# Kernel tuning notes

Measured on AMD Instinct MI355X. Metric: run time of the kernel, lower is better.

## Reference

```python
import jax, jax.numpy as jnp
import numpy as np


def _prelu(x, a):
    return jnp.where(x >= 0, x, a * x)


def _conv1x1(x, w, b, a):
    # x: [N,C,H,W], w: [O,C], b: [O] -> PReLU(conv1x1(x))
    y = jnp.einsum('oc,nchw->nohw', w, x) + b[None, :, None, None]
    return _prelu(y, a)


def setup_inputs() -> dict:
    key = jax.random.key(0)
    ks = jax.random.split(key, 8)
    N, C, H, W = 4, 128, 64, 64
    Cr = C // 2  # reduction=2
    sC = 1.0 / np.sqrt(C)
    x = jax.random.normal(ks[0], (N, C, H, W), dtype=jnp.float32)
    w1 = jax.random.normal(ks[1], (Cr, C), dtype=jnp.float32) * sC
    b1 = jnp.zeros((Cr,), dtype=jnp.float32)
    a1 = jnp.asarray(0.25, dtype=jnp.float32)  # PReLU (single shared slope)
    w2 = jax.random.normal(ks[2], (Cr, C), dtype=jnp.float32) * sC
    b2 = jnp.zeros((Cr,), dtype=jnp.float32)
    a2 = jnp.asarray(0.25, dtype=jnp.float32)
    wa = jax.random.normal(ks[3], (C, C), dtype=jnp.float32) * sC
    ba = jnp.zeros((C,), dtype=jnp.float32)
    aa = jnp.asarray(0.25, dtype=jnp.float32)
    return {"x": x, "w1": w1, "b1": b1, "a1": a1,
            "w2": w2, "b2": b2, "a2": a2,
            "wa": wa, "ba": ba, "aa": aa}


def reference(x, w1, b1, a1, w2, b2, a2, wa, ba, aa):
    N, C, H, W = x.shape
    HW = H * W
    e1 = _conv1x1(x, w1, b1, a1).reshape(N, -1, HW)   # [N,Cr,HW]
    e2 = _conv1x1(x, w2, b2, a2).reshape(N, -1, HW)   # [N,Cr,HW]
    asm = _conv1x1(x, wa, ba, aa).reshape(N, C, HW)   # [N,C,HW]
    # ksize=1: per-channel outer products summed over channels == single contraction
    score = jnp.einsum('nci,ncj->nij', e1, e2)        # [N,HW,HW]
    score = jax.nn.softmax(score, axis=2)
    out = jnp.einsum('nij,ncj->nci', score, asm)      # [N,C,HW]
    return out.reshape(N, C, H, W)
```

## Files before the change

kernel.cpp:

```cpp
#include <hip/hip_runtime.h>
#include <hip/hip_bf16.h>
#include <stdint.h>


typedef float   f32x16 __attribute__((ext_vector_type(16)));
typedef __bf16  bf16x8 __attribute__((ext_vector_type(8)));
typedef __bf16  bf16x2 __attribute__((ext_vector_type(2)));
typedef unsigned int u32x4 __attribute__((ext_vector_type(4)));
typedef unsigned int u32x2 __attribute__((ext_vector_type(2)));

#define L2E 1.4426950408889634f

#define Q_OFF   (0u)
#define KF_OFF  (2u << 20)
#define VF_OFF  (4u << 20)
#define DEN_OFF (8u << 20)
#define WH_OFF  ((8u << 20) + (1u << 19))
#define WL_OFF  (WH_OFF + (1u << 16))
#define OP_OFF  (9u << 20)

__device__ inline unsigned short f2bf(float f) {
  __bf16 h = (__bf16)f;
  return __builtin_bit_cast(unsigned short, h);
}
__device__ inline float bf2f(unsigned short h) {
  unsigned u = ((unsigned)h) << 16;
  return __builtin_bit_cast(float, u);
}
__device__ inline unsigned pack2(float a, float b) {
  bf16x2 t = { (__bf16)a, (__bf16)b };
  return __builtin_bit_cast(unsigned, t);
}

__device__ inline void gld_lds16(const void* g, void* l) {
  __builtin_amdgcn_global_load_lds(
      (const __attribute__((address_space(1))) unsigned*)g,
      (__attribute__((address_space(3))) unsigned*)l, 16, 0, 0);
}

__global__ void wcast_kernel(const float* __restrict__ w1, const float* __restrict__ w2,
                             const float* __restrict__ wa, char* __restrict__ ws) {
  int idx = blockIdx.x * 256 + threadIdx.x;
  unsigned short* WH = (unsigned short*)(ws + WH_OFF);
  unsigned short* WL = (unsigned short*)(ws + WL_OFF);
#pragma unroll
  for (int r = 0; r < 4; ++r) {
    int i = r * 8192 + idx;
    int oc = i >> 7, c = i & 127;
    float v = oc < 64 ? w1[oc * 128 + c]
            : (oc < 128 ? w2[(oc - 64) * 128 + c] : wa[(oc - 128) * 128 + c]);
    __bf16 h = (__bf16)v;
    WH[i] = __builtin_bit_cast(unsigned short, h);
    WL[i] = f2bf(v - (float)h);
  }
}

__global__ __launch_bounds__(256) void conv_kernel(
    const float* __restrict__ x, char* __restrict__ ws,
    const float* __restrict__ b1, const float* __restrict__ a1,
    const float* __restrict__ b2, const float* __restrict__ a2,
    const float* __restrict__ ba, const float* __restrict__ aa) {
  int bid = blockIdx.x;
  int n = bid >> 7, st = bid & 127;
  int sb = st * 32;
  int tid = threadIdx.x;
  int wid = tid >> 6, lane = tid & 63, l31 = lane & 31, hi = lane >> 5;

  __shared__ float xl[128][36];
  __shared__ float tl[2][64][33];
  float* vl = (float*)xl;

  const float* xb = x + (size_t)n * 128 * 4096;
#pragma unroll
  for (int it = 0; it < 4; ++it) {
    int flat4 = tid + 256 * it;
    int c = flat4 >> 3, s4 = flat4 & 7;
    float4 v = *(const float4*)(xb + (size_t)c * 4096 + sb + s4 * 4);
    *(float4*)&xl[c][s4 * 4] = v;
  }
  __syncthreads();

  const char* WH = ws + WH_OFF;
  const char* WL = ws + WL_OFF;
  int oc0 = wid * 64;

  f32x16 acc[2];
  acc[0] = 0.f; acc[1] = 0.f;
#pragma unroll
  for (int c0 = 0; c0 < 8; ++c0) {
    __bf16 eh[8], el[8];
#pragma unroll
    for (int j = 0; j < 8; ++j) {
      float v = xl[c0 * 16 + hi * 8 + j][l31];
      __bf16 h = (__bf16)v;
      eh[j] = h;
      el[j] = (__bf16)(v - (float)h);
    }
    bf16x8 xh = {eh[0], eh[1], eh[2], eh[3], eh[4], eh[5], eh[6], eh[7]};
    bf16x8 xlo = {el[0], el[1], el[2], el[3], el[4], el[5], el[6], el[7]};
#pragma unroll
    for (int mb = 0; mb < 2; ++mb) {
      size_t wo = (size_t)(oc0 + mb * 32 + l31) * 256 + c0 * 32 + hi * 16;
      bf16x8 wh = *(const bf16x8*)(WH + wo);
      bf16x8 wl = *(const bf16x8*)(WL + wo);
      acc[mb] = __builtin_amdgcn_mfma_f32_32x32x16_bf16(wh, xh, acc[mb], 0, 0, 0);
      acc[mb] = __builtin_amdgcn_mfma_f32_32x32x16_bf16(wh, xlo, acc[mb], 0, 0, 0);
      acc[mb] = __builtin_amdgcn_mfma_f32_32x32x16_bf16(wl, xh, acc[mb], 0, 0, 0);
    }
  }
  __syncthreads();

  if (wid < 2) {
    const float* bb = wid ? b2 : b1;
    float slope = wid ? a2[0] : a1[0];
    float scl = wid ? 1.0f : L2E;
#pragma unroll
    for (int mb = 0; mb < 2; ++mb)
#pragma unroll
      for (int reg = 0; reg < 16; ++reg) {
        int row = mb * 32 + (reg & 3) + 8 * (reg >> 2) + 4 * hi;
        float y = acc[mb][reg] + bb[row];
        y = fmaxf(y, 0.f) + slope * fminf(y, 0.f);
        tl[wid][row][l31] = y * scl;
      }
  } else {
    float slope = aa[0];
#pragma unroll
    for (int mb = 0; mb < 2; ++mb)
#pragma unroll
      for (int reg = 0; reg < 16; ++reg) {
        int dv = (wid - 2) * 64 + mb * 32 + (reg & 3) + 8 * (reg >> 2) + 4 * hi;
        float y = acc[mb][reg] + ba[dv];
        y = fmaxf(y, 0.f) + slope * fminf(y, 0.f);
        vl[dv * 33 + l31] = y;
      }
  }
  __syncthreads();

  if (wid == 0) {
    char* Qg = ws + Q_OFF + (size_t)n * (4096 * 128);
#pragma unroll
    for (int it = 0; it < 4; ++it) {
      int sl = (lane >> 3) + it * 8;
      u32x4 pv;
#pragma unroll
      for (int p = 0; p < 4; ++p)
        pv[p] = pack2(tl[0][(lane & 7) * 8 + 2 * p][sl],
                      tl[0][(lane & 7) * 8 + 2 * p + 1][sl]);
      *(u32x4*)(Qg + (size_t)(sb + sl) * 128 + (lane & 7) * 16) = pv;
    }
  } else if (wid == 1) {
    char* KFb = ws + KF_OFF + (size_t)n * (512 << 10);
    int d0 = (lane & 7) >> 1, hs = lane & 1;
#pragma unroll
    for (int it = 0; it < 4; ++it) {
      int sl = (lane >> 3) + it * 8;
      u32x4 pv;
#pragma unroll
      for (int p = 0; p < 4; ++p)
        pv[p] = pack2(tl[1][(lane & 7) * 8 + 2 * p][sl],
                      tl[1][(lane & 7) * 8 + 2 * p + 1][sl]);
      *(u32x4*)(KFb + ((size_t)(st * 4 + d0) * 64 + hs * 32 + sl) * 16) = pv;
    }
  }
  {
    char* VFb = ws + VF_OFF + (size_t)n * (1u << 20);
#pragma unroll
    for (int r = 0; r < 2; ++r) {
      int u = tid + r * 256;
      int dv = u >> 2, sc = u & 3;
      u32x4 pv;
#pragma unroll
      for (int p = 0; p < 4; ++p)
        pv[p] = pack2(vl[dv * 33 + sc * 8 + 2 * p], vl[dv * 33 + sc * 8 + 2 * p + 1]);
      int unit = st * 8 + (dv >> 5) * 2 + (sc >> 1);
      *(u32x4*)(VFb + ((size_t)unit * 64 + (sc & 1) * 32 + (dv & 31)) * 16) = pv;
    }
  }
}

__global__ __launch_bounds__(256, 2) void attn_kernel(char* __restrict__ ws) {
  int bid = blockIdx.x;
  int split = bid & 3;
  int qt = (bid >> 2) & 15;
  int batch = bid >> 6;
  int tid = threadIdx.x;
  int wid = tid >> 6, lane = tid & 63, l31 = lane & 31, hi = lane >> 5;

  const char* Qb  = ws + Q_OFF  + (size_t)batch * (4096 * 128);
  const char* Kt0 = ws + KF_OFF + (size_t)batch * (512 << 10) +
                    (size_t)(split * 32) * 4096;
  const char* Vt0 = ws + VF_OFF + (size_t)batch * (1u << 20) +
                    (size_t)(split * 32) * 8192;

  __shared__ char sbuf[3][12288];

  int q0 = qt * 256 + wid * 64;
  int lo16 = lane * 16;

  bf16x8 qf0[4], qf1[4];
#pragma unroll
  for (int d0 = 0; d0 < 4; ++d0) {
    qf0[d0] = *(const bf16x8*)(Qb + (size_t)(q0 + l31) * 128 + d0 * 32 + hi * 16);
    qf1[d0] = *(const bf16x8*)(Qb + (size_t)(q0 + 32 + l31) * 128 + d0 * 32 + hi * 16);
  }

  f32x16 oacc[2][4];
#pragma unroll
  for (int qs = 0; qs < 2; ++qs)
#pragma unroll
    for (int i = 0; i < 4; ++i) oacc[qs][i] = 0.f;
  float denA0 = 0.f, denA1 = 0.f, denB0 = 0.f, denB1 = 0.f;

  auto stage = [&](int b, int t) {
#pragma unroll
    for (int i = 0; i < 3; ++i) {
      int c = wid * 3 + i;
      const char* src = (c < 4) ? Kt0 + (size_t)t * 4096 + c * 1024 + lo16
                                : Vt0 + (size_t)t * 8192 + (c - 4) * 1024 + lo16;
      gld_lds16(src, &sbuf[b][c * 1024]);
    }
  };

  stage(0, 0);
  stage(1, 1);

  for (int t = 0; t < 32; ++t) {
    if (t < 31) asm volatile("s_waitcnt vmcnt(3)" ::: "memory");
    else        asm volatile("s_waitcnt vmcnt(0)" ::: "memory");
    __builtin_amdgcn_s_barrier();

    if (t + 2 < 32) stage((t + 2) % 3, t + 2);

    const char* kb = sbuf[t % 3];
    const char* vb = kb + 4096;

    f32x16 s0, s1;
    s0 = 0.f; s1 = 0.f;
#pragma unroll
    for (int d0 = 0; d0 < 4; ++d0) {
      bf16x8 kf = *(const bf16x8*)(kb + d0 * 1024 + lo16);
      s0 = __builtin_amdgcn_mfma_f32_32x32x16_bf16(kf, qf0[d0], s0, 0, 0, 0);
      s1 = __builtin_amdgcn_mfma_f32_32x32x16_bf16(kf, qf1[d0], s1, 0, 0, 0);
    }

    unsigned pk0[8], pk1[8];
#pragma unroll
    for (int m = 0; m < 8; ++m) {
      float a0 = __builtin_amdgcn_exp2f(s0[2 * m]);
      float a1 = __builtin_amdgcn_exp2f(s0[2 * m + 1]);
      if (m & 1) denA1 += a0 + a1; else denA0 += a0 + a1;
      pk0[m] = pack2(a0, a1);
      float b0 = __builtin_amdgcn_exp2f(s1[2 * m]);
      float b1 = __builtin_amdgcn_exp2f(s1[2 * m + 1]);
      if (m & 1) denB1 += b0 + b1; else denB0 += b0 + b1;
      pk1[m] = pack2(b0, b1);
    }

#pragma unroll
    for (int kc = 0; kc < 2; ++kc) {
      const int bs = kc * 4;
      u32x2 r0 = __builtin_amdgcn_permlane32_swap(pk0[bs + 0], pk0[bs + 2],
                                                  false, false);
      u32x2 r1 = __builtin_amdgcn_permlane32_swap(pk0[bs + 1], pk0[bs + 3],
                                                  false, false);
      u32x4 pu0 = {r0.x, r1.x, r0.y, r1.y};
      bf16x8 pf0 = __builtin_bit_cast(bf16x8, pu0);
      u32x2 r2 = __builtin_amdgcn_permlane32_swap(pk1[bs + 0], pk1[bs + 2],
                                                  false, false);
      u32x2 r3 = __builtin_amdgcn_permlane32_swap(pk1[bs + 1], pk1[bs + 3],
                                                  false, false);
      u32x4 pu1 = {r2.x, r3.x, r2.y, r3.y};
      bf16x8 pf1 = __builtin_bit_cast(bf16x8, pu1);
#pragma unroll
      for (int dvb = 0; dvb < 4; ++dvb) {
        bf16x8 vf = *(const bf16x8*)(vb + (dvb * 2 + kc) * 1024 + lo16);
        oacc[0][dvb] = __builtin_amdgcn_mfma_f32_32x32x16_bf16(vf, pf0,
                                                               oacc[0][dvb], 0, 0, 0);
        oacc[1][dvb] = __builtin_amdgcn_mfma_f32_32x32x16_bf16(vf, pf1,
                                                               oacc[1][dvb], 0, 0, 0);
      }
    }
  }

  unsigned short* OPu = (unsigned short*)(ws + OP_OFF) +
                        (size_t)((batch * 16 + qt) * 4 + split) * 32768;
#pragma unroll
  for (int qs = 0; qs < 2; ++qs) {
    int qloc = wid * 64 + qs * 32 + l31;
#pragma unroll
    for (int dvb = 0; dvb < 4; ++dvb)
#pragma unroll
      for (int reg = 0; reg < 16; ++reg) {
        int dv = dvb * 32 + (reg & 3) + 8 * (reg >> 2) + 4 * hi;
        OPu[dv * 256 + qloc] = f2bf(oacc[qs][dvb][reg]);
      }
    float den = qs ? (denB0 + denB1) : (denA0 + denA1);
    float dtot = den + __shfl_xor(den, 32, 64);
    if (hi == 0) {
      float* DEN = (float*)(ws + DEN_OFF) +
                   (size_t)((batch * 16 + qt) * 4 + split) * 256;
      DEN[qloc] = dtot;
    }
  }
}

__global__ __launch_bounds__(256) void combine_kernel(const char* __restrict__ ws,
                                                      float* __restrict__ out) {
  int idx8 = (blockIdx.x * 256 + threadIdx.x) * 8;
  int n = idx8 >> 19;
  int dv = (idx8 >> 12) & 127;
  int s0 = idx8 & 4095;
  int qt = s0 >> 8, ql = s0 & 255;
  const unsigned short* OPu = (const unsigned short*)(ws + OP_OFF);
  const float* DEN = (const float*)(ws + DEN_OFF);
  size_t pb = (size_t)((n * 16 + qt) * 4);
  float num[8], den[8];
#pragma unroll
  for (int j = 0; j < 8; ++j) { num[j] = 0.f; den[j] = 0.f; }
#pragma unroll
  for (int h = 0; h < 4; ++h) {
    bf16x8 v = *(const bf16x8*)(OPu + (pb + h) * 32768 + (size_t)dv * 256 + ql);
    const float* dp = DEN + (pb + h) * 256 + ql;
    float4 d0 = *(const float4*)dp;
    float4 d1 = *(const float4*)(dp + 4);
#pragma unroll
    for (int j = 0; j < 8; ++j) num[j] += (float)v[j];
    den[0] += d0.x; den[1] += d0.y; den[2] += d0.z; den[3] += d0.w;
    den[4] += d1.x; den[5] += d1.y; den[6] += d1.z; den[7] += d1.w;
  }
  float4 o0 = {num[0] / den[0], num[1] / den[1], num[2] / den[2], num[3] / den[3]};
  float4 o1 = {num[4] / den[4], num[5] / den[5], num[6] / den[6], num[7] / den[7]};
  *(float4*)&out[idx8] = o0;
  *(float4*)&out[idx8 + 4] = o1;
}

extern "C" void kernel_launch(void* const* d_in, const int* in_sizes, int n_in,
                              void* d_out, int out_size, void* d_ws, size_t ws_size,
                              hipStream_t stream) {
  (void)in_sizes; (void)n_in; (void)out_size; (void)ws_size;
  const float* x  = (const float*)d_in[0];
  const float* w1 = (const float*)d_in[1];
  const float* b1 = (const float*)d_in[2];
  const float* a1 = (const float*)d_in[3];
  const float* w2 = (const float*)d_in[4];
  const float* b2 = (const float*)d_in[5];
  const float* a2 = (const float*)d_in[6];
  const float* wa = (const float*)d_in[7];
  const float* ba = (const float*)d_in[8];
  const float* aa = (const float*)d_in[9];
  char* ws = (char*)d_ws;
  float* out = (float*)d_out;

  wcast_kernel<<<dim3(32), dim3(256), 0, stream>>>(w1, w2, wa, ws);
  conv_kernel<<<dim3(512), dim3(256), 0, stream>>>(x, ws, b1, a1, b2, a2, ba, aa);
  attn_kernel<<<dim3(256), dim3(256), 0, stream>>>(ws);
  combine_kernel<<<dim3(1024), dim3(256), 0, stream>>>(ws, out);
}
```

Measured before the change: 59.29 us.

## Fuse split-K combine into attention kernel via last-block atomic counter

Removes the separate combine kernel launch. Each attention block atomically increments a per-(batch,qtile) counter after writing its partial output, and the last of the four split blocks reduces the partials and normalizes by the summed denominators directly into the output. This saves a kernel launch and its tail, at the cost of a memset for the counters and a serialized reduction inside the last-arriving block, which may lengthen the attention kernel's tail.

New measurement: 148.5 us. 150% more time.

```diff
diff --git a/kernel.cpp b/kernel.cpp
--- a/kernel.cpp
+++ b/kernel.cpp
@@ -15,6 +15,7 @@
 #define KF_OFF  (2u << 20)
 #define VF_OFF  (4u << 20)
 #define DEN_OFF (8u << 20)
+#define CNT_OFF ((8u << 20) + (256u << 10))
 #define WH_OFF  ((8u << 20) + (1u << 19))
 #define WL_OFF  (WH_OFF + (1u << 16))
 #define OP_OFF  (9u << 20)
@@ -179,7 +180,8 @@
   }
 }
 
-__global__ __launch_bounds__(256, 2) void attn_kernel(char* __restrict__ ws) {
+__global__ __launch_bounds__(256, 2) void attn_kernel(char* __restrict__ ws,
+                                                      float* __restrict__ out) {
   int bid = blockIdx.x;
   int split = bid & 3;
   int qt = (bid >> 2) & 15;
@@ -194,6 +196,7 @@
                     (size_t)(split * 32) * 8192;
 
   __shared__ char sbuf[3][12288];
+  __shared__ int lastFlag;
 
   int q0 = qt * 256 + wid * 64;
   int lo16 = lane * 16;
@@ -283,8 +286,9 @@
     }
   }
 
+  int grp = batch * 16 + qt;
   unsigned short* OPu = (unsigned short*)(ws + OP_OFF) +
-                        (size_t)((batch * 16 + qt) * 4 + split) * 32768;
+                        (size_t)(grp * 4 + split) * 32768;
 #pragma unroll
   for (int qs = 0; qs < 2; ++qs) {
     int qloc = wid * 64 + qs * 32 + l31;
@@ -298,41 +302,49 @@
     float den = qs ? (denB0 + denB1) : (denA0 + denA1);
     float dtot = den + __shfl_xor(den, 32, 64);
     if (hi == 0) {
-      float* DEN = (float*)(ws + DEN_OFF) +
-                   (size_t)((batch * 16 + qt) * 4 + split) * 256;
+      float* DEN = (float*)(ws + DEN_OFF) + (size_t)(grp * 4 + split) * 256;
       DEN[qloc] = dtot;
     }
   }
-}
-
-__global__ __launch_bounds__(256) void combine_kernel(const char* __restrict__ ws,
-                                                      float* __restrict__ out) {
-  int idx8 = (blockIdx.x * 256 + threadIdx.x) * 8;
-  int n = idx8 >> 19;
-  int dv = (idx8 >> 12) & 127;
-  int s0 = idx8 & 4095;
-  int qt = s0 >> 8, ql = s0 & 255;
-  const unsigned short* OPu = (const unsigned short*)(ws + OP_OFF);
-  const float* DEN = (const float*)(ws + DEN_OFF);
-  size_t pb = (size_t)((n * 16 + qt) * 4);
-  float num[8], den[8];
-#pragma unroll
-  for (int j = 0; j < 8; ++j) { num[j] = 0.f; den[j] = 0.f; }
-#pragma unroll
-  for (int h = 0; h < 4; ++h) {
-    bf16x8 v = *(const bf16x8*)(OPu + (pb + h) * 32768 + (size_t)dv * 256 + ql);
-    const float* dp = DEN + (pb + h) * 256 + ql;
-    float4 d0 = *(const float4*)dp;
-    float4 d1 = *(const float4*)(dp + 4);
-#pragma unroll
-    for (int j = 0; j < 8; ++j) num[j] += (float)v[j];
-    den[0] += d0.x; den[1] += d0.y; den[2] += d0.z; den[3] += d0.w;
-    den[4] += d1.x; den[5] += d1.y; den[6] += d1.z; den[7] += d1.w;
-  }
-  float4 o0 = {num[0] / den[0], num[1] / den[1], num[2] / den[2], num[3] / den[3]};
-  float4 o1 = {num[4] / den[4], num[5] / den[5], num[6] / den[6], num[7] / den[7]};
-  *(float4*)&out[idx8] = o0;
-  *(float4*)&out[idx8 + 4] = o1;
+
+  __threadfence();
+  if (tid == 0) {
+    unsigned* cnt = (unsigned*)(ws + CNT_OFF);
+    unsigned old = atomicAdd(&cnt[grp], 1u);
+    lastFlag = (old == 3u) ? 1 : 0;
+  }
+  __syncthreads();
+  if (lastFlag) {
+    __threadfence();
+    const unsigned short* OPg = (const unsigned short*)(ws + OP_OFF) +
+                                (size_t)grp * 4 * 32768;
+    const float* DENg = (const float*)(ws + DEN_OFF) + (size_t)grp * 4 * 256;
+    int dv = tid >> 1;
+    int qlb = (tid & 1) * 128;
+    float* og = out + ((size_t)batch * 128 + dv) * 4096 + qt * 256 + qlb;
+#pragma unroll
+    for (int u = 0; u < 16; ++u) {
+      int ql = qlb + u * 8;
+      float num[8], den[8];
+#pragma unroll
+      for (int j = 0; j < 8; ++j) { num[j] = 0.f; den[j] = 0.f; }
+#pragma unroll
+      for (int sp = 0; sp < 4; ++sp) {
+        bf16x8 v = *(const bf16x8*)(OPg + sp * 32768 + dv * 256 + ql);
+        const float* dp = DENg + sp * 256 + ql;
+        float4 d0 = *(const float4*)dp;
+        float4 d1 = *(const float4*)(dp + 4);
+#pragma unroll
+        for (int j = 0; j < 8; ++j) num[j] += (float)v[j];
+        den[0] += d0.x; den[1] += d0.y; den[2] += d0.z; den[3] += d0.w;
+        den[4] += d1.x; den[5] += d1.y; den[6] += d1.z; den[7] += d1.w;
+      }
+      float4 o0 = {num[0] / den[0], num[1] / den[1], num[2] / den[2], num[3] / den[3]};
+      float4 o1 = {num[4] / den[4], num[5] / den[5], num[6] / den[6], num[7] / den[7]};
+      *(float4*)(og + u * 8) = o0;
+      *(float4*)(og + u * 8 + 4) = o1;
+    }
+  }
 }
 
 extern "C" void kernel_launch(void* const* d_in, const int* in_sizes, int n_in,
@@ -352,8 +364,8 @@
   char* ws = (char*)d_ws;
   float* out = (float*)d_out;
 
+  hipMemsetAsync(ws + CNT_OFF, 0, 64 * sizeof(unsigned), stream);
   wcast_kernel<<<dim3(32), dim3(256), 0, stream>>>(w1, w2, wa, ws);
   conv_kernel<<<dim3(512), dim3(256), 0, stream>>>(x, ws, b1, a1, b2, a2, ba, aa);
-  attn_kernel<<<dim3(256), dim3(256), 0, stream>>>(ws);
-  combine_kernel<<<dim3(1024), dim3(256), 0, stream>>>(ws, out);
-}
+  attn_kernel<<<dim3(256), dim3(256), 0, stream>>>(ws, out);
+}
```

## Split keys across warps within a block and fuse the combine step into attention

Applied to the files above, without the earlier changes.

Each block now covers one 64-query tile. Its four warps each process a quarter of the key range with private triple-buffered LDS staging, so the per-iteration block barrier goes away. The partial numerators and denominators are reduced through shared memory at the end, and the normalized output is written directly. This removes the separate combine kernel launch and the global round-trip of bf16 partials. In exchange the kernel uses 144KB of LDS, so occupancy drops to one block per CU with only four waves. Each warp also issues its own K/V loads, which quadruples LDS fill traffic per block.

Result: slower. 61.08 us (+3.0%).

```diff
diff --git a/kernel.cpp b/kernel.cpp
--- a/kernel.cpp
+++ b/kernel.cpp
@@ -14,10 +14,8 @@
 #define Q_OFF   (0u)
 #define KF_OFF  (2u << 20)
 #define VF_OFF  (4u << 20)
-#define DEN_OFF (8u << 20)
 #define WH_OFF  ((8u << 20) + (1u << 19))
 #define WL_OFF  (WH_OFF + (1u << 16))
-#define OP_OFF  (9u << 20)
 
 __device__ inline unsigned short f2bf(float f) {
   __bf16 h = (__bf16)f;
@@ -179,23 +177,24 @@
   }
 }
 
-__global__ __launch_bounds__(256, 2) void attn_kernel(char* __restrict__ ws) {
+__global__ __launch_bounds__(256, 1) void attn_kernel(char* __restrict__ ws,
+                                                      float* __restrict__ out) {
   int bid = blockIdx.x;
-  int split = bid & 3;
-  int qt = (bid >> 2) & 15;
-  int batch = bid >> 6;
+  int batch = bid & 3;
+  int qt = bid >> 2;
   int tid = threadIdx.x;
   int wid = tid >> 6, lane = tid & 63, l31 = lane & 31, hi = lane >> 5;
 
   const char* Qb  = ws + Q_OFF  + (size_t)batch * (4096 * 128);
   const char* Kt0 = ws + KF_OFF + (size_t)batch * (512 << 10) +
-                    (size_t)(split * 32) * 4096;
+                    (size_t)(wid * 32) * 4096;
   const char* Vt0 = ws + VF_OFF + (size_t)batch * (1u << 20) +
-                    (size_t)(split * 32) * 8192;
-
-  __shared__ char sbuf[3][12288];
-
-  int q0 = qt * 256 + wid * 64;
+                    (size_t)(wid * 32) * 8192;
+
+  __shared__ char sbuf[4][3][12288];
+  char* myb = &sbuf[wid][0][0];
+
+  int q0 = qt * 64;
   int lo16 = lane * 16;
 
   bf16x8 qf0[4], qf1[4];
@@ -213,26 +212,26 @@
   float denA0 = 0.f, denA1 = 0.f, denB0 = 0.f, denB1 = 0.f;
 
   auto stage = [&](int b, int t) {
-#pragma unroll
-    for (int i = 0; i < 3; ++i) {
-      int c = wid * 3 + i;
-      const char* src = (c < 4) ? Kt0 + (size_t)t * 4096 + c * 1024 + lo16
-                                : Vt0 + (size_t)t * 8192 + (c - 4) * 1024 + lo16;
-      gld_lds16(src, &sbuf[b][c * 1024]);
-    }
+    char* dst = myb + b * 12288;
+    const char* ks = Kt0 + (size_t)t * 4096;
+    const char* vs = Vt0 + (size_t)t * 8192;
+#pragma unroll
+    for (int i = 0; i < 4; ++i) gld_lds16(ks + i * 1024 + lo16, dst + i * 1024);
+#pragma unroll
+    for (int i = 0; i < 8; ++i) gld_lds16(vs + i * 1024 + lo16,
+                                          dst + 4096 + i * 1024);
   };
 
   stage(0, 0);
   stage(1, 1);
 
   for (int t = 0; t < 32; ++t) {
-    if (t < 31) asm volatile("s_waitcnt vmcnt(3)" ::: "memory");
+    if (t < 31) asm volatile("s_waitcnt vmcnt(12)" ::: "memory");
     else        asm volatile("s_waitcnt vmcnt(0)" ::: "memory");
-    __builtin_amdgcn_s_barrier();
 
     if (t + 2 < 32) stage((t + 2) % 3, t + 2);
 
-    const char* kb = sbuf[t % 3];
+    const char* kb = myb + (t % 3) * 12288;
     const char* vb = kb + 4096;
 
     f32x16 s0, s1;
@@ -283,56 +282,49 @@
     }
   }
 
-  unsigned short* OPu = (unsigned short*)(ws + OP_OFF) +
-                        (size_t)((batch * 16 + qt) * 4 + split) * 32768;
+  __syncthreads();
+
+  unsigned short* pOP = (unsigned short*)&sbuf[0][0][0];
+  float* pDEN = (float*)((char*)pOP + 4 * 64 * 136 * 2);
+
 #pragma unroll
   for (int qs = 0; qs < 2; ++qs) {
-    int qloc = wid * 64 + qs * 32 + l31;
+    int q = qs * 32 + l31;
 #pragma unroll
     for (int dvb = 0; dvb < 4; ++dvb)
 #pragma unroll
-      for (int reg = 0; reg < 16; ++reg) {
-        int dv = dvb * 32 + (reg & 3) + 8 * (reg >> 2) + 4 * hi;
-        OPu[dv * 256 + qloc] = f2bf(oacc[qs][dvb][reg]);
+      for (int j = 0; j < 4; ++j) {
+        int db = dvb * 32 + 8 * j + 4 * hi;
+        u32x2 wv = { pack2(oacc[qs][dvb][4 * j],     oacc[qs][dvb][4 * j + 1]),
+                     pack2(oacc[qs][dvb][4 * j + 2], oacc[qs][dvb][4 * j + 3]) };
+        *(u32x2*)&pOP[(wid * 64 + q) * 136 + db] = wv;
       }
     float den = qs ? (denB0 + denB1) : (denA0 + denA1);
     float dtot = den + __shfl_xor(den, 32, 64);
-    if (hi == 0) {
-      float* DEN = (float*)(ws + DEN_OFF) +
-                   (size_t)((batch * 16 + qt) * 4 + split) * 256;
-      DEN[qloc] = dtot;
-    }
-  }
-}
-
-__global__ __launch_bounds__(256) void combine_kernel(const char* __restrict__ ws,
-                                                      float* __restrict__ out) {
-  int idx8 = (blockIdx.x * 256 + threadIdx.x) * 8;
-  int n = idx8 >> 19;
-  int dv = (idx8 >> 12) & 127;
-  int s0 = idx8 & 4095;
-  int qt = s0 >> 8, ql = s0 & 255;
-  const unsigned short* OPu = (const unsigned short*)(ws + OP_OFF);
-  const float* DEN = (const float*)(ws + DEN_OFF);
-  size_t pb = (size_t)((n * 16 + qt) * 4);
-  float num[8], den[8];
-#pragma unroll
-  for (int j = 0; j < 8; ++j) { num[j] = 0.f; den[j] = 0.f; }
-#pragma unroll
-  for (int h = 0; h < 4; ++h) {
-    bf16x8 v = *(const bf16x8*)(OPu + (pb + h) * 32768 + (size_t)dv * 256 + ql);
-    const float* dp = DEN + (pb + h) * 256 + ql;
-    float4 d0 = *(const float4*)dp;
-    float4 d1 = *(const float4*)(dp + 4);
-#pragma unroll
-    for (int j = 0; j < 8; ++j) num[j] += (float)v[j];
-    den[0] += d0.x; den[1] += d0.y; den[2] += d0.z; den[3] += d0.w;
-    den[4] += d1.x; den[5] += d1.y; den[6] += d1.z; den[7] += d1.w;
-  }
-  float4 o0 = {num[0] / den[0], num[1] / den[1], num[2] / den[2], num[3] / den[3]};
-  float4 o1 = {num[4] / den[4], num[5] / den[5], num[6] / den[6], num[7] / den[7]};
-  *(float4*)&out[idx8] = o0;
-  *(float4*)&out[idx8 + 4] = o1;
+    if (hi == 0) pDEN[wid * 64 + q] = dtot;
+  }
+  __syncthreads();
+
+  {
+    int q = tid & 63, dvg = tid >> 6;
+    float dsum = (pDEN[q] + pDEN[64 + q]) + (pDEN[128 + q] + pDEN[192 + q]);
+    float inv = 1.0f / dsum;
+    float* og = out + (size_t)batch * 128 * 4096 + (size_t)qt * 64 + q;
+#pragma unroll
+    for (int it = 0; it < 4; ++it) {
+      int dv = dvg * 32 + it * 8;
+      float acc8[8] = {0.f, 0.f, 0.f, 0.f, 0.f, 0.f, 0.f, 0.f};
+#pragma unroll
+      for (int w = 0; w < 4; ++w) {
+        bf16x8 v = *(const bf16x8*)&pOP[(w * 64 + q) * 136 + dv];
+#pragma unroll
+        for (int j = 0; j < 8; ++j) acc8[j] += (float)v[j];
+      }
+#pragma unroll
+      for (int j = 0; j < 8; ++j)
+        og[(size_t)(dv + j) * 4096] = acc8[j] * inv;
+    }
+  }
 }
 
 extern "C" void kernel_launch(void* const* d_in, const int* in_sizes, int n_in,
@@ -354,6 +346,5 @@
 
   wcast_kernel<<<dim3(32), dim3(256), 0, stream>>>(w1, w2, wa, ws);
   conv_kernel<<<dim3(512), dim3(256), 0, stream>>>(x, ws, b1, a1, b2, a2, ba, aa);
-  attn_kernel<<<dim3(256), dim3(256), 0, stream>>>(ws);
-  combine_kernel<<<dim3(1024), dim3(256), 0, stream>>>(ws, out);
-}
+  attn_kernel<<<dim3(256), dim3(256), 0, stream>>>(ws, out);
+}
```

## Split attention KV range across two wave groups per block with LDS reduction

Applied to the files above, without the earlier changes.

Doubles the attention block to 512 threads, with two groups of four waves each processing half of the split's key/value tiles in separate LDS ring buffers. At the end, the second group writes its partial outputs (as bf16) and denominators to LDS, and the first group adds them before storing. The aim is to shorten the serial per-wave loop and raise wave count per block on a 256-block grid that may underfill the GPU. In exchange it adds an LDS reduction, extra barriers, doubled LDS use, and a bf16 rounding of the partial sums.

Result: no change. 59.98 us (+1.2%).

```diff
diff --git a/kernel.cpp b/kernel.cpp
--- a/kernel.cpp
+++ b/kernel.cpp
@@ -179,23 +179,26 @@
   }
 }
 
-__global__ __launch_bounds__(256, 2) void attn_kernel(char* __restrict__ ws) {
+__global__ __launch_bounds__(512, 1) void attn_kernel(char* __restrict__ ws) {
   int bid = blockIdx.x;
   int split = bid & 3;
   int qt = (bid >> 2) & 15;
   int batch = bid >> 6;
   int tid = threadIdx.x;
-  int wid = tid >> 6, lane = tid & 63, l31 = lane & 31, hi = lane >> 5;
+  int wid = tid >> 6;
+  int kvh = wid & 1, qc = wid >> 1;
+  int lane = tid & 63, l31 = lane & 31, hi = lane >> 5;
 
   const char* Qb  = ws + Q_OFF  + (size_t)batch * (4096 * 128);
   const char* Kt0 = ws + KF_OFF + (size_t)batch * (512 << 10) +
-                    (size_t)(split * 32) * 4096;
+                    (size_t)(split * 32 + kvh * 16) * 4096;
   const char* Vt0 = ws + VF_OFF + (size_t)batch * (1u << 20) +
-                    (size_t)(split * 32) * 8192;
-
-  __shared__ char sbuf[3][12288];
-
-  int q0 = qt * 256 + wid * 64;
+                    (size_t)(split * 32 + kvh * 16) * 8192;
+
+  __shared__ __align__(16) char sbuf[2][3][12288];
+  char* myb = &sbuf[kvh][0][0];
+
+  int q0 = qt * 256 + qc * 64;
   int lo16 = lane * 16;
 
   bf16x8 qf0[4], qf1[4];
@@ -215,24 +218,24 @@
   auto stage = [&](int b, int t) {
 #pragma unroll
     for (int i = 0; i < 3; ++i) {
-      int c = wid * 3 + i;
+      int c = qc * 3 + i;
       const char* src = (c < 4) ? Kt0 + (size_t)t * 4096 + c * 1024 + lo16
                                 : Vt0 + (size_t)t * 8192 + (c - 4) * 1024 + lo16;
-      gld_lds16(src, &sbuf[b][c * 1024]);
+      gld_lds16(src, &myb[b * 12288 + c * 1024]);
     }
   };
 
   stage(0, 0);
   stage(1, 1);
 
-  for (int t = 0; t < 32; ++t) {
-    if (t < 31) asm volatile("s_waitcnt vmcnt(3)" ::: "memory");
+  for (int t = 0; t < 16; ++t) {
+    if (t < 15) asm volatile("s_waitcnt vmcnt(3)" ::: "memory");
     else        asm volatile("s_waitcnt vmcnt(0)" ::: "memory");
     __builtin_amdgcn_s_barrier();
 
-    if (t + 2 < 32) stage((t + 2) % 3, t + 2);
-
-    const char* kb = sbuf[t % 3];
+    if (t + 2 < 16) stage((t + 2) % 3, t + 2);
+
+    const char* kb = myb + (t % 3) * 12288;
     const char* vb = kb + 4096;
 
     f32x16 s0, s1;
@@ -283,24 +286,60 @@
     }
   }
 
-  unsigned short* OPu = (unsigned short*)(ws + OP_OFF) +
-                        (size_t)((batch * 16 + qt) * 4 + split) * 32768;
-#pragma unroll
-  for (int qs = 0; qs < 2; ++qs) {
-    int qloc = wid * 64 + qs * 32 + l31;
-#pragma unroll
-    for (int dvb = 0; dvb < 4; ++dvb)
-#pragma unroll
-      for (int reg = 0; reg < 16; ++reg) {
-        int dv = dvb * 32 + (reg & 3) + 8 * (reg >> 2) + 4 * hi;
-        OPu[dv * 256 + qloc] = f2bf(oacc[qs][dvb][reg]);
-      }
-    float den = qs ? (denB0 + denB1) : (denA0 + denA1);
-    float dtot = den + __shfl_xor(den, 32, 64);
-    if (hi == 0) {
-      float* DEN = (float*)(ws + DEN_OFF) +
-                   (size_t)((batch * 16 + qt) * 4 + split) * 256;
-      DEN[qloc] = dtot;
+  float myden[2] = {denA0 + denA1, denB0 + denB1};
+#pragma unroll
+  for (int qs = 0; qs < 2; ++qs)
+    myden[qs] += __shfl_xor(myden[qs], 32, 64);
+
+  __syncthreads();
+  u32x2* xch = (u32x2*)&sbuf[0][0][0];
+  float* denx = (float*)((char*)xch + 65536);
+
+  if (kvh == 1) {
+#pragma unroll
+    for (int qs = 0; qs < 2; ++qs) {
+#pragma unroll
+      for (int dvb = 0; dvb < 4; ++dvb)
+#pragma unroll
+        for (int j = 0; j < 4; ++j) {
+          int idx = ((qc * 2 + qs) * 4 + dvb) * 4 + j;
+          u32x2 wv = { pack2(oacc[qs][dvb][4 * j],     oacc[qs][dvb][4 * j + 1]),
+                       pack2(oacc[qs][dvb][4 * j + 2], oacc[qs][dvb][4 * j + 3]) };
+          xch[idx * 64 + lane] = wv;
+        }
+      denx[(qc * 2 + qs) * 64 + lane] = myden[qs];
+    }
+  }
+  __syncthreads();
+
+  if (kvh == 0) {
+    int grp = batch * 16 + qt;
+    unsigned short* OPu = (unsigned short*)(ws + OP_OFF) +
+                          (size_t)(grp * 4 + split) * 32768;
+    float* DEN = (float*)(ws + DEN_OFF) + (size_t)(grp * 4 + split) * 256;
+#pragma unroll
+    for (int qs = 0; qs < 2; ++qs) {
+#pragma unroll
+      for (int dvb = 0; dvb < 4; ++dvb)
+#pragma unroll
+        for (int j = 0; j < 4; ++j) {
+          int idx = ((qc * 2 + qs) * 4 + dvb) * 4 + j;
+          u32x2 wv = xch[idx * 64 + lane];
+          oacc[qs][dvb][4 * j]     += bf2f((unsigned short)(wv.x & 0xffffu));
+          oacc[qs][dvb][4 * j + 1] += bf2f((unsigned short)(wv.x >> 16));
+          oacc[qs][dvb][4 * j + 2] += bf2f((unsigned short)(wv.y & 0xffffu));
+          oacc[qs][dvb][4 * j + 3] += bf2f((unsigned short)(wv.y >> 16));
+        }
+      int qloc = qc * 64 + qs * 32 + l31;
+#pragma unroll
+      for (int dvb = 0; dvb < 4; ++dvb)
+#pragma unroll
+        for (int reg = 0; reg < 16; ++reg) {
+          int dv = dvb * 32 + (reg & 3) + 8 * (reg >> 2) + 4 * hi;
+          OPu[dv * 256 + qloc] = f2bf(oacc[qs][dvb][reg]);
+        }
+      if (hi == 0)
+        DEN[qloc] = myden[qs] + denx[(qc * 2 + qs) * 64 + lane];
     }
   }
 }
@@ -354,6 +393,6 @@
 
   wcast_kernel<<<dim3(32), dim3(256), 0, stream>>>(w1, w2, wa, ws);
   conv_kernel<<<dim3(512), dim3(256), 0, stream>>>(x, ws, b1, a1, b2, a2, ba, aa);
-  attn_kernel<<<dim3(256), dim3(256), 0, stream>>>(ws);
+  attn_kernel<<<dim3(256), dim3(512), 0, stream>>>(ws);
   combine_kernel<<<dim3(1024), dim3(256), 0, stream>>>(ws, out);
 }
```
